# Optimization experiments

Measured on AMD Instinct MI355X. Metric: run time of the kernel, lower is better.

## Reference

```python
import jax, jax.numpy as jnp
import numpy as np
from jax import lax

GRID_N = 80
C_FEAT = 128
HID = 256
NLAYERS = 12


def _make_grid_mesh(n):
    xs = np.linspace(-0.9, 0.9, n, dtype=np.float32)
    X, Y = np.meshgrid(xs, xs, indexing='xy')
    verts = np.stack([X.ravel(), Y.ravel(), np.zeros(n * n, np.float32)], 1)
    idx = np.arange(n * n).reshape(n, n)
    a = idx[:-1, :-1].ravel(); b = idx[:-1, 1:].ravel()
    c = idx[1:, :-1].ravel(); d = idx[1:, 1:].ravel()
    faces = np.concatenate([np.stack([a, b, c], 1), np.stack([b, d, c], 1)], 0)
    return verts, faces.astype(np.int64)


def _edges_and_inv(faces):
    F = faces.shape[0]
    e = np.concatenate([faces[:, [0, 1]], faces[:, [1, 2]], faces[:, [2, 0]]], 0)
    e = np.sort(e, 1)
    edges, inv = np.unique(e, axis=0, return_inverse=True)
    inv = inv.reshape(-1)
    return edges.astype(np.int32), inv[:F], inv[F:2 * F], inv[2 * F:]


def _subdivide_faces(faces, V):
    # new vertex k is midpoint of unique edge k, placed at index V + k
    edges, i01, i12, i20 = _edges_and_inv(faces)
    m01 = V + i01; m12 = V + i12; m20 = V + i20
    v0, v1, v2 = faces[:, 0], faces[:, 1], faces[:, 2]
    nf = np.concatenate([np.stack([v0, m01, m20], 1), np.stack([v1, m12, m01], 1),
                         np.stack([v2, m20, m12], 1), np.stack([m01, m12, m20], 1)], 0)
    return edges, nf


def _topology():
    verts0, f1 = _make_grid_mesh(GRID_N)
    V1 = verts0.shape[0]
    edges1, f2 = _subdivide_faces(f1, V1)
    V2 = V1 + edges1.shape[0]
    edges2, f3 = _subdivide_faces(f2, V2)
    V3 = V2 + edges2.shape[0]
    edges3 = _edges_and_inv(f3)[0]
    return verts0, edges1, edges2, edges3, V3


def _vert_align(feat, verts):
    # feat [C,H,W]; sample bilinearly at vertex (x,y) in [-1,1], align_corners, zero padding
    C, H, W = feat.shape
    fx = (verts[:, 0] + 1.0) * 0.5 * (W - 1)
    fy = (verts[:, 1] + 1.0) * 0.5 * (H - 1)
    x0 = jnp.floor(fx); y0 = jnp.floor(fy)
    wx = fx - x0; wy = fy - y0
    x0i = x0.astype(jnp.int32); y0i = y0.astype(jnp.int32)
    fT = jnp.transpose(feat, (1, 2, 0))  # [H,W,C]

    def samp(yi, xi):
        valid = ((yi >= 0) & (yi < H) & (xi >= 0) & (xi < W)).astype(feat.dtype)
        v = fT[jnp.clip(yi, 0, H - 1), jnp.clip(xi, 0, W - 1)]
        return v * valid[:, None]

    return (samp(y0i, x0i) * ((1 - wy) * (1 - wx))[:, None]
            + samp(y0i, x0i + 1) * ((1 - wy) * wx)[:, None]
            + samp(y0i + 1, x0i) * (wy * (1 - wx))[:, None]
            + samp(y0i + 1, x0i + 1) * (wy * wx)[:, None])


def _gconv(x, e0, e1, w, b):
    # pytorch3d GraphConv: w0(x) + sum_{j in N(i)} w1(x_j), undirected edges
    h0 = x @ w[0] + b[0]
    h1 = x @ w[1] + b[1]
    agg = jnp.zeros_like(h0).at[e0].add(h1[e1]).at[e1].add(h1[e0])
    return h0 + agg


def _stage(feat, edges, w_in, b_in, w_h, b_h, w_out, b_out):
    e0, e1 = edges[:, 0], edges[:, 1]
    x = _gconv(feat, e0, e1, w_in, b_in)

    def body(xc, p):
        return _gconv(xc, e0, e1, p[0], p[1]), None

    x, _ = lax.scan(body, x, (w_h, b_h))
    coords = _gconv(x, e0, e1, w_out, b_out)
    return x, coords


def _subdiv(f, edges):
    # SubdivideMeshes feature/vertex rule: append edge midpoints
    return jnp.concatenate([f, 0.5 * (f[edges[:, 0]] + f[edges[:, 1]])], 0)


def setup_inputs() -> dict:
    key = jax.random.key(0)
    ks = jax.random.split(key, 16)
    verts0, edges1, edges2, edges3, V3 = _topology()

    def pw(k, din, dout, L=None):
        shape = (L, 2, din, dout) if L else (2, din, dout)
        return jax.random.normal(k, shape, dtype=jnp.float32) / np.float32(np.sqrt(7.0 * din))

    din2 = C_FEAT + HID
    inp = {
        'conv64': jax.random.normal(ks[0], (C_FEAT, 56, 56), jnp.float32),
        'conv128': jax.random.normal(ks[1], (C_FEAT, 28, 28), jnp.float32),
        'conv256': jax.random.normal(ks[2], (C_FEAT, 14, 14), jnp.float32),
        'verts0': jnp.asarray(verts0),
        'edges1': jnp.asarray(edges1), 'edges2': jnp.asarray(edges2), 'edges3': jnp.asarray(edges3),
        'w_in1': pw(ks[3], C_FEAT, HID), 'b_in1': jnp.zeros((2, HID), jnp.float32),
        'w_h1': pw(ks[4], HID, HID, NLAYERS), 'b_h1': jnp.zeros((NLAYERS, 2, HID), jnp.float32),
        'w_out1': pw(ks[5], HID, 3), 'b_out1': jnp.zeros((2, 3), jnp.float32),
        'w_in2': pw(ks[6], din2, HID), 'b_in2': jnp.zeros((2, HID), jnp.float32),
        'w_h2': pw(ks[7], HID, HID, NLAYERS), 'b_h2': jnp.zeros((NLAYERS, 2, HID), jnp.float32),
        'w_out2': pw(ks[8], HID, 3), 'b_out2': jnp.zeros((2, 3), jnp.float32),
        'w_in3': pw(ks[9], din2, HID), 'b_in3': jnp.zeros((2, HID), jnp.float32),
        'w_h3': pw(ks[10], HID, HID, NLAYERS), 'b_h3': jnp.zeros((NLAYERS, 2, HID), jnp.float32),
        'w_out3': pw(ks[11], HID, 3), 'b_out3': jnp.zeros((2, 3), jnp.float32),
    }
    return inp


def reference(conv64, conv128, conv256, verts0,
              w_in1, b_in1, w_h1, b_h1, w_out1, b_out1,
              w_in2, b_in2, w_h2, b_h2, w_out2, b_out2,
              w_in3, b_in3, w_h3, b_h3, w_out3, b_out3,
              edges1, edges2, edges3):
    # stage 1: vert_align on conv64 + 14 graph convs -> coords
    x, c1 = _stage(_vert_align(conv64, verts0), edges1, w_in1, b_in1, w_h1, b_h1, w_out1, b_out1)
    v2 = _subdiv(c1, edges1)
    h2 = _subdiv(x, edges1)
    f2 = jnp.concatenate([_vert_align(conv128, v2), h2], 1)
    x, c2 = _stage(f2, edges2, w_in2, b_in2, w_h2, b_h2, w_out2, b_out2)
    v3 = _subdiv(c2, edges2)
    h3 = _subdiv(x, edges2)
    f3 = jnp.concatenate([_vert_align(conv256, v3), h3], 1)
    _, c3 = _stage(f3, edges3, w_in3, b_in3, w_h3, b_h3, w_out3, b_out3)
    return c3
```

## Files before the change

kernel.cpp:

```cpp
#include <hip/hip_runtime.h>
#include <utility>

#define HID 256

typedef __attribute__((ext_vector_type(8))) short bf16x8;
typedef __attribute__((ext_vector_type(4))) float f32x4;
typedef __attribute__((ext_vector_type(4))) unsigned short us4;
typedef __attribute__((ext_vector_type(8))) unsigned short us8;

constexpr size_t MAXN3 = 100489;
constexpr size_t MAXE3 = 300200;

constexpr size_t OFF_IN1 = 0;
constexpr size_t OFF_IN2 = OFF_IN1 + 2 * 256 * 128;
constexpr size_t OFF_IN3 = OFF_IN2 + 2 * 256 * 384;
constexpr size_t OFF_H1  = OFF_IN3 + 2 * 256 * 384;
constexpr size_t OFF_H2  = OFF_H1 + 24 * 256 * 256;
constexpr size_t OFF_H3  = OFF_H2 + 24 * 256 * 256;
constexpr size_t WT_TOTAL = OFF_H3 + 24 * 256 * 256;

__device__ __attribute__((aligned(16))) unsigned short g_Ah[MAXN3 * 256];
__device__ __attribute__((aligned(16))) unsigned short g_Al[MAXN3 * 256];
__device__ __attribute__((aligned(16))) unsigned short g_Bh[MAXN3 * 256];
__device__ __attribute__((aligned(16))) unsigned short g_Bl[MAXN3 * 256];
__device__ __attribute__((aligned(16))) unsigned short g_Gh[MAXN3 * 256];
__device__ __attribute__((aligned(16))) unsigned short g_Gl[MAXN3 * 256];
__device__ __attribute__((aligned(16))) unsigned short g_Dh[MAXN3 * 256];
__device__ __attribute__((aligned(16))) unsigned short g_Dl[MAXN3 * 256];
__device__ __attribute__((aligned(16))) unsigned short g_VAh[MAXN3 * 128];
__device__ __attribute__((aligned(16))) unsigned short g_VAl[MAXN3 * 128];
__device__ float g_C0[MAXN3 * 3];
__device__ float g_C2[MAXN3 * 3];
__device__ float g_Vv[MAXN3 * 3];
__device__ float g_T [56 * 56 * 128];
__device__ __attribute__((aligned(16))) unsigned short g_Wth[WT_TOTAL];
__device__ __attribute__((aligned(16))) unsigned short g_Wtl[WT_TOTAL];
__device__ int g_deg   [MAXN3];
__device__ int g_rowptr[MAXN3 + 1];
__device__ int g_cursor[MAXN3];
__device__ int g_adj   [2 * MAXE3];
__device__ int g_bsum  [128];

__device__ inline float b2f(unsigned short h) {
  return __uint_as_float((unsigned)h << 16);
}
__device__ inline void fsplit(float f, unsigned short& h, unsigned short& l) {
  unsigned u = __float_as_uint(f);
  h = (unsigned short)(u >> 16);
  float hf = __uint_as_float(u & 0xffff0000u);
  l = (unsigned short)(__float_as_uint(f - hf) >> 16);
}

#define GLOAD16(g, l)                                                       \
  __builtin_amdgcn_global_load_lds(                                        \
      (const __attribute__((address_space(1))) unsigned*)(const void*)(g), \
      (__attribute__((address_space(3))) unsigned*)(void*)(l), 16, 0, 0)

__global__ __launch_bounds__(256) void k_wtrans(const float* __restrict__ W,
                                                unsigned short* __restrict__ Oh,
                                                unsigned short* __restrict__ Ol,
                                                int K) {
  __shared__ float Ls[64][65];
  int ktb = blockIdx.x, cb = blockIdx.y, mat = blockIdx.z;
  int nktb = gridDim.x;
  const float* Wm = W + (size_t)mat * K * 256;
  int t = threadIdx.x;
#pragma unroll
  for (int i = 0; i < 16; ++i) {
    int idx = i * 256 + t;
    int kk = idx >> 6, cc = idx & 63;
    Ls[kk][cc] = Wm[(size_t)(ktb * 64 + kk) * 256 + cb * 64 + cc];
  }
  __syncthreads();
  size_t tb = ((size_t)(mat * 4 + cb) * nktb + ktb) * 4096;
#pragma unroll
  for (int i = 0; i < 2; ++i) {
    int c = t * 2 + i;
    int n = c >> 3, sp = c & 7;
    int kbase = (sp ^ (n & 7)) * 8;
    unsigned short hb[8], lb[8];
#pragma unroll
    for (int j = 0; j < 8; ++j) {
      float v = Ls[kbase + j][n];
      unsigned short hi, lo;
      fsplit(v, hi, lo);
      hb[j] = hi;
      lb[j] = lo;
    }
    *(us4*)(Oh + tb + c * 8)     = (us4){hb[0], hb[1], hb[2], hb[3]};
    *(us4*)(Oh + tb + c * 8 + 4) = (us4){hb[4], hb[5], hb[6], hb[7]};
    *(us4*)(Ol + tb + c * 8)     = (us4){lb[0], lb[1], lb[2], lb[3]};
    *(us4*)(Ol + tb + c * 8 + 4) = (us4){lb[4], lb[5], lb[6], lb[7]};
  }
}


__global__ __launch_bounds__(256) void k_count(const int* __restrict__ edges,
                                               int* __restrict__ deg, int E) {
  int e = blockIdx.x * blockDim.x + threadIdx.x;
  if (e >= E) return;
  atomicAdd(&deg[edges[2 * e + 0]], 1);
  atomicAdd(&deg[edges[2 * e + 1]], 1);
}

__global__ __launch_bounds__(256) void k_scan_part(const int* __restrict__ deg,
                                                   int* __restrict__ bsum, int N) {
  __shared__ int s[256];
  int t = threadIdx.x;
  int base = blockIdx.x * 1024 + t * 4;
  int v = 0;
#pragma unroll
  for (int i = 0; i < 4; ++i) {
    int idx = base + i;
    if (idx < N) v += deg[idx];
  }
  s[t] = v;
  __syncthreads();
  for (int off = 128; off > 0; off >>= 1) {
    if (t < off) s[t] += s[t + off];
    __syncthreads();
  }
  if (t == 0) bsum[blockIdx.x] = s[0];
}

__global__ __launch_bounds__(128) void k_scan_top(int* __restrict__ bsum, int nb) {
  __shared__ int s[128];
  int t = threadIdx.x;
  s[t] = (t < nb) ? bsum[t] : 0;
  __syncthreads();
  for (int off = 1; off < 128; off <<= 1) {
    int v = (t >= off) ? s[t - off] : 0;
    __syncthreads();
    s[t] += v;
    __syncthreads();
  }
  if (t < nb) bsum[t] = (t == 0) ? 0 : s[t - 1];
}

__global__ __launch_bounds__(256) void k_scan_write(const int* __restrict__ deg,
                                                    const int* __restrict__ bsum,
                                                    int* __restrict__ rowptr,
                                                    int* __restrict__ cursor, int N) {
  __shared__ int s[256];
  int t = threadIdx.x;
  int base = blockIdx.x * 1024;
  int d[4];
  int local = 0;
#pragma unroll
  for (int i = 0; i < 4; ++i) {
    int idx = base + t * 4 + i;
    d[i] = (idx < N) ? deg[idx] : 0;
    local += d[i];
  }
  s[t] = local;
  __syncthreads();
  for (int off = 1; off < 256; off <<= 1) {
    int v = (t >= off) ? s[t - off] : 0;
    __syncthreads();
    s[t] += v;
    __syncthreads();
  }
  int run = bsum[blockIdx.x] + s[t] - local;
#pragma unroll
  for (int i = 0; i < 4; ++i) {
    int idx = base + t * 4 + i;
    if (idx < N) {
      rowptr[idx] = run;
      cursor[idx] = run;
    }
    run += d[i];
  }
  if (blockIdx.x == gridDim.x - 1 && t == 255) rowptr[N] = run;
}

__global__ __launch_bounds__(256) void k_fill(const int* __restrict__ edges,
                                              int* __restrict__ cursor,
                                              int* __restrict__ adj, int E) {
  int e = blockIdx.x * blockDim.x + threadIdx.x;
  if (e >= E) return;
  int a = edges[2 * e + 0];
  int b = edges[2 * e + 1];
  adj[atomicAdd(&cursor[a], 1)] = b;
  adj[atomicAdd(&cursor[b], 1)] = a;
}


__global__ __launch_bounds__(128) void k_transpose(const float* __restrict__ in,
                                                   float* __restrict__ out, int HW) {
  int p = blockIdx.x;
  int c = threadIdx.x;
  if (p < HW) out[(size_t)p * 128 + c] = in[(size_t)c * HW + p];
}

__global__ __launch_bounds__(128) void k_vert_align(const float* __restrict__ fT,
                                                    const float* __restrict__ verts,
                                                    unsigned short* __restrict__ oh,
                                                    unsigned short* __restrict__ ol,
                                                    int N, int H, int W) {
  int v = blockIdx.x;
  if (v >= N) return;
  int c = threadIdx.x;
  float vx = verts[(size_t)v * 3 + 0];
  float vy = verts[(size_t)v * 3 + 1];
  float fx = (vx + 1.f) * 0.5f * (float)(W - 1);
  float fy = (vy + 1.f) * 0.5f * (float)(H - 1);
  float x0f = floorf(fx), y0f = floorf(fy);
  float wx = fx - x0f, wy = fy - y0f;
  int x0 = (int)x0f, y0 = (int)y0f;
  float acc = 0.f;
#pragma unroll
  for (int dy = 0; dy < 2; ++dy) {
#pragma unroll
    for (int dx = 0; dx < 2; ++dx) {
      int yi = y0 + dy, xi = x0 + dx;
      bool valid = (yi >= 0) && (yi < H) && (xi >= 0) && (xi < W);
      int yc = min(max(yi, 0), H - 1);
      int xc = min(max(xi, 0), W - 1);
      float val = fT[((size_t)yc * W + xc) * 128 + c];
      float wgt = (dy ? wy : 1.f - wy) * (dx ? wx : 1.f - wx);
      acc += valid ? val * wgt : 0.f;
    }
  }
  unsigned short h, l;
  fsplit(acc, h, l);
  oh[(size_t)v * 128 + c] = h;
  ol[(size_t)v * 128 + c] = l;
}

template <int CH>
__global__ __launch_bounds__(256) void k_gather(const int* __restrict__ rowptr,
                                                const int* __restrict__ adj,
                                                const unsigned short* __restrict__ Xh,
                                                const unsigned short* __restrict__ Xl,
                                                unsigned short* __restrict__ Gh,
                                                unsigned short* __restrict__ Gl, int N) {
  constexpr int TPV = CH / 8;
  int idx = blockIdx.x * blockDim.x + threadIdx.x;
  int v = idx / TPV;
  if (v >= N) return;
  int c = (idx % TPV) * 8;
  float a[8] = {};
  int lo = rowptr[v], hi = rowptr[v + 1];
  for (int i = lo; i < hi; ++i) {
    size_t base = (size_t)adj[i] * CH + c;
    us8 h = *(const us8*)(Xh + base);
    us8 l = *(const us8*)(Xl + base);
#pragma unroll
    for (int j = 0; j < 8; ++j) a[j] += b2f(h[j]) + b2f(l[j]);
  }
  us8 oh, ol;
#pragma unroll
  for (int j = 0; j < 8; ++j) {
    unsigned short hh, ll;
    fsplit(a[j], hh, ll);
    oh[j] = hh;
    ol[j] = ll;
  }
  *(us8*)(Gh + (size_t)v * CH + c) = oh;
  *(us8*)(Gl + (size_t)v * CH + c) = ol;
}

struct Panels {
  const unsigned short* ph[4];
  const unsigned short* pl[4];
  int ks[4];
  int ld[4];
};

#define SWZ(row, slot) (((row) * 64) + (((slot) ^ ((row) & 7)) << 3))

__global__ __launch_bounds__(256, 2) void k_layer(
    Panels pd, int Kmm,
    const unsigned short* __restrict__ w0h, const unsigned short* __restrict__ w0l,
    const unsigned short* __restrict__ w1h, const unsigned short* __restrict__ w1l,
    int Kw,
    const float* __restrict__ b0, const float* __restrict__ b1,
    const int* __restrict__ deg,
    unsigned short* __restrict__ Yh, unsigned short* __restrict__ Yl, int N) {
  __shared__ __attribute__((aligned(16))) unsigned short Xh_lds[128 * 64];
  __shared__ __attribute__((aligned(16))) unsigned short Xl_lds[128 * 64];
  __shared__ __attribute__((aligned(16))) unsigned short Wh_lds[2 * 4096];
  __shared__ __attribute__((aligned(16))) unsigned short Wl_lds[2 * 4096];
  int tid = threadIdx.x;
  int lane = tid & 63;
  int wid = tid >> 6;
  int wm = wid >> 1;
  int wn = wid & 1;

  int nrt = (N + 127) >> 7;
  int total = nrt * 2;
  int flat = blockIdx.x;
  int rowtile, colblk;
  if ((flat & ~15) + 16 <= total) {
    int sub = flat & 15;
    rowtile = (flat >> 4) * 8 + (sub & 7);
    colblk = sub >> 3;
  } else {
    rowtile = flat >> 1;
    colblk = flat & 1;
  }
  int row0 = rowtile * 128;
  int col0 = colblk * 128;
  int nktbw = Kw >> 6;

  f32x4 acc[4][4];
#pragma unroll
  for (int m = 0; m < 4; ++m)
#pragma unroll
    for (int n = 0; n < 4; ++n) acc[m][n] = (f32x4){0.f, 0.f, 0.f, 0.f};

  for (int kt = 0; kt < Kmm; kt += 64) {
    int pi = (kt >= pd.ks[1]) + (kt >= pd.ks[2]) + (kt >= pd.ks[3]);
    const unsigned short* bph = pd.ph[pi];
    const unsigned short* bpl = pd.pl[pi];
    int ld = pd.ld[pi];
    int koff = kt - pd.ks[pi];
#pragma unroll
    for (int i = 0; i < 4; ++i) {
      int c = (wid * 4 + i) * 64 + lane;
      int row = c >> 3, slot = c & 7;
      int vg = min(row0 + row, N - 1);
      size_t so = (size_t)vg * ld + koff + ((slot ^ (row & 7)) << 3);
      GLOAD16(bph + so, &Xh_lds[(size_t)c * 8]);
      GLOAD16(bpl + so, &Xl_lds[(size_t)c * 8]);
    }
    {
      int ktb = (kt < Kw) ? (kt >> 6) : ((kt - Kw) >> 6);
      const unsigned short* mh = (kt < Kw) ? w0h : w1h;
      const unsigned short* ml = (kt < Kw) ? w0l : w1l;
#pragma unroll
      for (int i = 0; i < 4; ++i) {
        int c = (wid * 4 + i) * 64 + lane;
        int half = c >> 9, ci = c & 511;
        size_t tb = ((size_t)((2 * colblk + half) * nktbw + ktb)) * 4096 + (size_t)ci * 8;
        GLOAD16(mh + tb, &Wh_lds[half * 4096 + ci * 8]);
        GLOAD16(ml + tb, &Wl_lds[half * 4096 + ci * 8]);
      }
    }
    __syncthreads();
#pragma unroll
    for (int ks = 0; ks < 2; ++ks) {
      int slot = ks * 4 + (lane >> 4);
      bf16x8 ah[4], al[4];
#pragma unroll
      for (int m = 0; m < 4; ++m) {
        int row = wm * 64 + m * 16 + (lane & 15);
        int off = SWZ(row, slot);
        ah[m] = *(const bf16x8*)&Xh_lds[off];
        al[m] = *(const bf16x8*)&Xl_lds[off];
      }
      bf16x8 bh[4], bl[4];
#pragma unroll
      for (int n = 0; n < 4; ++n) {
        int nr = n * 16 + (lane & 15);
        int off = wn * 4096 + SWZ(nr, slot);
        bh[n] = *(const bf16x8*)&Wh_lds[off];
        bl[n] = *(const bf16x8*)&Wl_lds[off];
      }
#pragma unroll
      for (int m = 0; m < 4; ++m)
#pragma unroll
        for (int n = 0; n < 4; ++n) {
          f32x4 c = acc[m][n];
          c = __builtin_amdgcn_mfma_f32_16x16x32_bf16(al[m], bh[n], c, 0, 0, 0);
          c = __builtin_amdgcn_mfma_f32_16x16x32_bf16(ah[m], bl[n], c, 0, 0, 0);
          c = __builtin_amdgcn_mfma_f32_16x16x32_bf16(ah[m], bh[n], c, 0, 0, 0);
          acc[m][n] = c;
        }
    }
    __syncthreads();
  }

#pragma unroll
  for (int m = 0; m < 4; ++m) {
    int rbase = row0 + wm * 64 + m * 16 + (lane >> 4) * 4;
    float dv[4];
#pragma unroll
    for (int r = 0; r < 4; ++r)
      dv[r] = (rbase + r < N) ? (float)deg[rbase + r] : 0.f;
#pragma unroll
    for (int n = 0; n < 4; ++n) {
      int col = col0 + wn * 64 + n * 16 + (lane & 15);
      float bb0 = b0[col], bb1 = b1[col];
      f32x4 v = acc[m][n];
#pragma unroll
      for (int r = 0; r < 4; ++r) {
        int row = rbase + r;
        if (row < N) {
          unsigned short h, l;
          fsplit(v[r] + bb0 + dv[r] * bb1, h, l);
          Yh[(size_t)row * HID + col] = h;
          Yl[(size_t)row * HID + col] = l;
        }
      }
    }
  }
}

__global__ __launch_bounds__(256) void k_rowdot6(const unsigned short* __restrict__ Xh,
                                                 const unsigned short* __restrict__ Xl,
                                                 const float* __restrict__ W,
                                                 const float* __restrict__ b,
                                                 float* __restrict__ Y0,
                                                 float* __restrict__ Y1, int N) {
  int gid = blockIdx.x * blockDim.x + threadIdx.x;
  int row = gid >> 6;
  int lane = threadIdx.x & 63;
  if (row >= N) return;
  size_t base = (size_t)row * HID + lane * 4;
  us4 hv = *(const us4*)(Xh + base);
  us4 lv = *(const us4*)(Xl + base);
  float s[6] = {0.f, 0.f, 0.f, 0.f, 0.f, 0.f};
#pragma unroll
  for (int k = 0; k < 4; ++k) {
    float x = b2f(hv[k]) + b2f(lv[k]);
    int kk = lane * 4 + k;
#pragma unroll
    for (int j = 0; j < 3; ++j) {
      s[j]     += x * W[kk * 3 + j];
      s[3 + j] += x * W[768 + kk * 3 + j];
    }
  }
#pragma unroll
  for (int off = 32; off > 0; off >>= 1)
#pragma unroll
    for (int j = 0; j < 6; ++j) s[j] += __shfl_down(s[j], off);
  if (lane == 0) {
#pragma unroll
    for (int j = 0; j < 3; ++j) {
      Y0[(size_t)row * 3 + j] = s[j] + b[j];
      Y1[(size_t)row * 3 + j] = s[3 + j] + b[3 + j];
    }
  }
}

__global__ __launch_bounds__(256) void k_scatter3(const int* __restrict__ edges,
                                                  const float* __restrict__ H,
                                                  float* __restrict__ OUT, int E) {
  int e = blockIdx.x * blockDim.x + threadIdx.x;
  if (e >= E) return;
  int a = edges[(size_t)e * 2 + 0];
  int b = edges[(size_t)e * 2 + 1];
#pragma unroll
  for (int k = 0; k < 3; ++k) {
    atomicAdd(&OUT[(size_t)a * 3 + k], H[(size_t)b * 3 + k]);
    atomicAdd(&OUT[(size_t)b * 3 + k], H[(size_t)a * 3 + k]);
  }
}

__global__ __launch_bounds__(256) void k_subdiv3(const float* __restrict__ c,
                                                 const int* __restrict__ edges,
                                                 float* __restrict__ v, int N, int E) {
  int i = blockIdx.x * blockDim.x + threadIdx.x;
  if (i >= N + E) return;
  if (i < N) {
#pragma unroll
    for (int k = 0; k < 3; ++k) v[(size_t)i * 3 + k] = c[(size_t)i * 3 + k];
  } else {
    int e = i - N;
    int a = edges[(size_t)e * 2 + 0];
    int b = edges[(size_t)e * 2 + 1];
#pragma unroll
    for (int k = 0; k < 3; ++k)
      v[(size_t)i * 3 + k] = 0.5f * (c[(size_t)a * 3 + k] + c[(size_t)b * 3 + k]);
  }
}

__global__ __launch_bounds__(256) void k_subdiv_feat(const unsigned short* __restrict__ xh,
                                                     const unsigned short* __restrict__ xl,
                                                     const int* __restrict__ edges,
                                                     unsigned short* __restrict__ oh,
                                                     unsigned short* __restrict__ ol,
                                                     int N, int E) {
  int idx = blockIdx.x * blockDim.x + threadIdx.x;
  int v = idx >> 5;
  if (v >= N + E) return;
  int c = (idx & 31) * 8;
  us8 rh, rl;
  if (v < N) {
    rh = *(const us8*)(xh + (size_t)v * HID + c);
    rl = *(const us8*)(xl + (size_t)v * HID + c);
  } else {
    int e = v - N;
    int a = edges[(size_t)e * 2 + 0];
    int b = edges[(size_t)e * 2 + 1];
    us8 ahv = *(const us8*)(xh + (size_t)a * HID + c);
    us8 alv = *(const us8*)(xl + (size_t)a * HID + c);
    us8 bhv = *(const us8*)(xh + (size_t)b * HID + c);
    us8 blv = *(const us8*)(xl + (size_t)b * HID + c);
#pragma unroll
    for (int j = 0; j < 8; ++j) {
      float f = 0.5f * ((b2f(ahv[j]) + b2f(alv[j])) + (b2f(bhv[j]) + b2f(blv[j])));
      unsigned short hh, ll;
      fsplit(f, hh, ll);
      rh[j] = hh;
      rl[j] = ll;
    }
  }
  *(us8*)(oh + (size_t)v * HID + c) = rh;
  *(us8*)(ol + (size_t)v * HID + c) = rl;
}


extern "C" void kernel_launch(void* const* d_in, const int* in_sizes, int n_in,
                              void* d_out, int out_size, void* d_ws, size_t ws_size,
                              hipStream_t stream) {
  const float* conv64  = (const float*)d_in[0];
  const float* conv128 = (const float*)d_in[1];
  const float* conv256 = (const float*)d_in[2];
  const float* verts0  = (const float*)d_in[3];
  const int*   edges1  = (const int*)d_in[4];
  const int*   edges2  = (const int*)d_in[5];
  const int*   edges3  = (const int*)d_in[6];
  const float* w_in1 = (const float*)d_in[7],  *b_in1 = (const float*)d_in[8];
  const float* w_h1  = (const float*)d_in[9],  *b_h1  = (const float*)d_in[10];
  const float* w_out1= (const float*)d_in[11], *b_out1= (const float*)d_in[12];
  const float* w_in2 = (const float*)d_in[13], *b_in2 = (const float*)d_in[14];
  const float* w_h2  = (const float*)d_in[15], *b_h2  = (const float*)d_in[16];
  const float* w_out2= (const float*)d_in[17], *b_out2= (const float*)d_in[18];
  const float* w_in3 = (const float*)d_in[19], *b_in3 = (const float*)d_in[20];
  const float* w_h3  = (const float*)d_in[21], *b_h3  = (const float*)d_in[22];
  const float* w_out3= (const float*)d_in[23], *b_out3= (const float*)d_in[24];

  const int N1 = in_sizes[3] / 3;
  const int E1 = in_sizes[4] / 2;
  const int E2 = in_sizes[5] / 2;
  const int E3 = in_sizes[6] / 2;
  const int N2 = N1 + E1;
  const int N3 = N2 + E2;
  if ((size_t)N3 > MAXN3 || (size_t)E3 > MAXE3) return;

  unsigned short *Ah, *Al, *Bh, *Bl, *Gh, *Gl, *Dh, *Dl, *VAh, *VAl;
  float *C0, *C2, *Vv, *T;
  unsigned short *Wth, *Wtl;
  int *deg, *rowptr, *cursor, *adj, *bsum;
  hipGetSymbolAddress((void**)&Ah,  HIP_SYMBOL(g_Ah));
  hipGetSymbolAddress((void**)&Al,  HIP_SYMBOL(g_Al));
  hipGetSymbolAddress((void**)&Bh,  HIP_SYMBOL(g_Bh));
  hipGetSymbolAddress((void**)&Bl,  HIP_SYMBOL(g_Bl));
  hipGetSymbolAddress((void**)&Gh,  HIP_SYMBOL(g_Gh));
  hipGetSymbolAddress((void**)&Gl,  HIP_SYMBOL(g_Gl));
  hipGetSymbolAddress((void**)&Dh,  HIP_SYMBOL(g_Dh));
  hipGetSymbolAddress((void**)&Dl,  HIP_SYMBOL(g_Dl));
  hipGetSymbolAddress((void**)&VAh, HIP_SYMBOL(g_VAh));
  hipGetSymbolAddress((void**)&VAl, HIP_SYMBOL(g_VAl));
  hipGetSymbolAddress((void**)&C0, HIP_SYMBOL(g_C0));
  hipGetSymbolAddress((void**)&C2, HIP_SYMBOL(g_C2));
  hipGetSymbolAddress((void**)&Vv, HIP_SYMBOL(g_Vv));
  hipGetSymbolAddress((void**)&T,  HIP_SYMBOL(g_T));
  hipGetSymbolAddress((void**)&Wth, HIP_SYMBOL(g_Wth));
  hipGetSymbolAddress((void**)&Wtl, HIP_SYMBOL(g_Wtl));
  hipGetSymbolAddress((void**)&deg,    HIP_SYMBOL(g_deg));
  hipGetSymbolAddress((void**)&rowptr, HIP_SYMBOL(g_rowptr));
  hipGetSymbolAddress((void**)&cursor, HIP_SYMBOL(g_cursor));
  hipGetSymbolAddress((void**)&adj,    HIP_SYMBOL(g_adj));
  hipGetSymbolAddress((void**)&bsum,   HIP_SYMBOL(g_bsum));

  k_wtrans<<<dim3(2, 4, 2),  256, 0, stream>>>(w_in1, Wth + OFF_IN1, Wtl + OFF_IN1, 128);
  k_wtrans<<<dim3(6, 4, 2),  256, 0, stream>>>(w_in2, Wth + OFF_IN2, Wtl + OFF_IN2, 384);
  k_wtrans<<<dim3(6, 4, 2),  256, 0, stream>>>(w_in3, Wth + OFF_IN3, Wtl + OFF_IN3, 384);
  k_wtrans<<<dim3(4, 4, 24), 256, 0, stream>>>(w_h1,  Wth + OFF_H1,  Wtl + OFF_H1,  256);
  k_wtrans<<<dim3(4, 4, 24), 256, 0, stream>>>(w_h2,  Wth + OFF_H2,  Wtl + OFF_H2,  256);
  k_wtrans<<<dim3(4, 4, 24), 256, 0, stream>>>(w_h3,  Wth + OFF_H3,  Wtl + OFF_H3,  256);

  const int BIG = 0x7fffffff;

  auto layerGrid = [](int N) { return dim3((unsigned)(((N + 127) / 128) * 2)); };

  auto build_csr = [&](const int* edges, int E, int N) {
    hipMemsetAsync(deg, 0, (size_t)N * sizeof(int), stream);
    k_count<<<(E + 255) / 256, 256, 0, stream>>>(edges, deg, E);
    int nb = (N + 1023) / 1024;
    k_scan_part<<<nb, 256, 0, stream>>>(deg, bsum, N);
    k_scan_top<<<1, 128, 0, stream>>>(bsum, nb);
    k_scan_write<<<nb, 256, 0, stream>>>(deg, bsum, rowptr, cursor, N);
    k_fill<<<(E + 255) / 256, 256, 0, stream>>>(edges, cursor, adj, E);
  };

  auto gconv_hidden = [&](size_t offH, const float* bh, int N) {
    unsigned short *Xh = Ah, *Xl = Al, *Yh = Bh, *Yl = Bl;
    for (int l = 0; l < 12; ++l) {
      const unsigned short* w0h = Wth + offH + (size_t)(2 * l + 0) * 65536;
      const unsigned short* w0l = Wtl + offH + (size_t)(2 * l + 0) * 65536;
      const unsigned short* w1h = Wth + offH + (size_t)(2 * l + 1) * 65536;
      const unsigned short* w1l = Wtl + offH + (size_t)(2 * l + 1) * 65536;
      const float* b0 = bh + (size_t)l * 2 * HID;
      const float* b1 = b0 + HID;
      k_gather<256><<<((size_t)N * 32 + 255) / 256, 256, 0, stream>>>(
          rowptr, adj, Xh, Xl, Gh, Gl, N);
      Panels pd = {{Xh, Gh, nullptr, nullptr}, {Xl, Gl, nullptr, nullptr},
                   {0, 256, BIG, BIG}, {256, 256, 0, 0}};
      k_layer<<<layerGrid(N), 256, 0, stream>>>(pd, 512, w0h, w0l, w1h, w1l, 256,
                                                b0, b1, deg, Yh, Yl, N);
      std::swap(Xh, Yh);
      std::swap(Xl, Yl);
    }
  };

  auto gconv_out = [&](const unsigned short* Xh, const unsigned short* Xl,
                       const float* wo, const float* bo,
                       float* Cdst, const int* edges, int E, int N) {
    k_rowdot6<<<((size_t)N * 64 + 255) / 256, 256, 0, stream>>>(Xh, Xl, wo, bo, Cdst, C2, N);
    k_scatter3<<<(E + 255) / 256, 256, 0, stream>>>(edges, C2, Cdst, E);
  };

  build_csr(edges1, E1, N1);
  k_transpose<<<56 * 56, 128, 0, stream>>>(conv64, T, 56 * 56);
  k_vert_align<<<N1, 128, 0, stream>>>(T, verts0, VAh, VAl, N1, 56, 56);
  k_gather<128><<<((size_t)N1 * 16 + 255) / 256, 256, 0, stream>>>(
      rowptr, adj, VAh, VAl, Gh, Gl, N1);
  {
    Panels pd = {{VAh, Gh, nullptr, nullptr}, {VAl, Gl, nullptr, nullptr},
                 {0, 128, BIG, BIG}, {128, 128, 0, 0}};
    k_layer<<<layerGrid(N1), 256, 0, stream>>>(pd, 256,
        Wth + OFF_IN1, Wtl + OFF_IN1, Wth + OFF_IN1 + 32768, Wtl + OFF_IN1 + 32768, 128,
        b_in1, b_in1 + HID, deg, Ah, Al, N1);
  }
  gconv_hidden(OFF_H1, b_h1, N1);
  gconv_out(Ah, Al, w_out1, b_out1, C0, edges1, E1, N1);
  k_subdiv3<<<(N2 + 255) / 256, 256, 0, stream>>>(C0, edges1, Vv, N1, E1);
  k_subdiv_feat<<<((size_t)N2 * 32 + 255) / 256, 256, 0, stream>>>(
      Ah, Al, edges1, Dh, Dl, N1, E1);

  build_csr(edges2, E2, N2);
  k_transpose<<<28 * 28, 128, 0, stream>>>(conv128, T, 28 * 28);
  k_vert_align<<<N2, 128, 0, stream>>>(T, Vv, VAh, VAl, N2, 28, 28);
  k_gather<128><<<((size_t)N2 * 16 + 255) / 256, 256, 0, stream>>>(
      rowptr, adj, VAh, VAl, Gh, Gl, N2);
  k_gather<256><<<((size_t)N2 * 32 + 255) / 256, 256, 0, stream>>>(
      rowptr, adj, Dh, Dl, Bh, Bl, N2);
  {
    const size_t m0 = OFF_IN2, m1 = OFF_IN2 + (size_t)256 * 384;
    Panels pd = {{VAh, Dh, Gh, Bh}, {VAl, Dl, Gl, Bl},
                 {0, 128, 384, 512}, {128, 256, 128, 256}};
    k_layer<<<layerGrid(N2), 256, 0, stream>>>(pd, 768,
        Wth + m0, Wtl + m0, Wth + m1, Wtl + m1, 384,
        b_in2, b_in2 + HID, deg, Ah, Al, N2);
  }
  gconv_hidden(OFF_H2, b_h2, N2);
  gconv_out(Ah, Al, w_out2, b_out2, C0, edges2, E2, N2);
  k_subdiv3<<<(N3 + 255) / 256, 256, 0, stream>>>(C0, edges2, Vv, N2, E2);
  k_subdiv_feat<<<((size_t)N3 * 32 + 255) / 256, 256, 0, stream>>>(
      Ah, Al, edges2, Dh, Dl, N2, E2);

  build_csr(edges3, E3, N3);
  k_transpose<<<14 * 14, 128, 0, stream>>>(conv256, T, 14 * 14);
  k_vert_align<<<N3, 128, 0, stream>>>(T, Vv, VAh, VAl, N3, 14, 14);
  k_gather<128><<<((size_t)N3 * 16 + 255) / 256, 256, 0, stream>>>(
      rowptr, adj, VAh, VAl, Gh, Gl, N3);
  k_gather<256><<<((size_t)N3 * 32 + 255) / 256, 256, 0, stream>>>(
      rowptr, adj, Dh, Dl, Bh, Bl, N3);
  {
    const size_t m0 = OFF_IN3, m1 = OFF_IN3 + (size_t)256 * 384;
    Panels pd = {{VAh, Dh, Gh, Bh}, {VAl, Dl, Gl, Bl},
                 {0, 128, 384, 512}, {128, 256, 128, 256}};
    k_layer<<<layerGrid(N3), 256, 0, stream>>>(pd, 768,
        Wth + m0, Wtl + m0, Wth + m1, Wtl + m1, 384,
        b_in3, b_in3 + HID, deg, Ah, Al, N3);
  }
  gconv_hidden(OFF_H3, b_h3, N3);
  float* OUT = (float*)d_out;
  k_rowdot6<<<((size_t)N3 * 64 + 255) / 256, 256, 0, stream>>>(
      Ah, Al, w_out3, b_out3, OUT, C2, N3);
  k_scatter3<<<(E3 + 255) / 256, 256, 0, stream>>>(edges3, C2, OUT, E3);
}
```

Baseline: 4.070 ms.

## Double-buffer GEMM LDS tiles with K=32 steps and matching weight layout

The layer GEMM now runs K in 32-wide steps with two LDS buffers, so the async global-to-LDS loads for the next tile are issued before computing on the current one, and one barrier per step replaces two. The weight pre-transform kernel is rewritten to emit 32-wide K blocks with a new 4-slot swizzle that matches the smaller tile. Total LDS use stays the same. The trade is half as many MFMAs per barrier and a changed swizzle pattern that could add bank conflicts.

```diff
diff --git a/kernel.cpp b/kernel.cpp
--- a/kernel.cpp
+++ b/kernel.cpp
@@ -60,38 +60,35 @@
                                                 unsigned short* __restrict__ Oh,
                                                 unsigned short* __restrict__ Ol,
                                                 int K) {
-  __shared__ float Ls[64][65];
+  __shared__ float Ls[32][65];
   int ktb = blockIdx.x, cb = blockIdx.y, mat = blockIdx.z;
   int nktb = gridDim.x;
   const float* Wm = W + (size_t)mat * K * 256;
   int t = threadIdx.x;
 #pragma unroll
-  for (int i = 0; i < 16; ++i) {
+  for (int i = 0; i < 8; ++i) {
     int idx = i * 256 + t;
     int kk = idx >> 6, cc = idx & 63;
-    Ls[kk][cc] = Wm[(size_t)(ktb * 64 + kk) * 256 + cb * 64 + cc];
+    Ls[kk][cc] = Wm[(size_t)(ktb * 32 + kk) * 256 + cb * 64 + cc];
   }
   __syncthreads();
-  size_t tb = ((size_t)(mat * 4 + cb) * nktb + ktb) * 4096;
-#pragma unroll
-  for (int i = 0; i < 2; ++i) {
-    int c = t * 2 + i;
-    int n = c >> 3, sp = c & 7;
-    int kbase = (sp ^ (n & 7)) * 8;
-    unsigned short hb[8], lb[8];
-#pragma unroll
-    for (int j = 0; j < 8; ++j) {
-      float v = Ls[kbase + j][n];
-      unsigned short hi, lo;
-      fsplit(v, hi, lo);
-      hb[j] = hi;
-      lb[j] = lo;
-    }
-    *(us4*)(Oh + tb + c * 8)     = (us4){hb[0], hb[1], hb[2], hb[3]};
-    *(us4*)(Oh + tb + c * 8 + 4) = (us4){hb[4], hb[5], hb[6], hb[7]};
-    *(us4*)(Ol + tb + c * 8)     = (us4){lb[0], lb[1], lb[2], lb[3]};
-    *(us4*)(Ol + tb + c * 8 + 4) = (us4){lb[4], lb[5], lb[6], lb[7]};
-  }
+  size_t tb = ((size_t)(mat * 4 + cb) * nktb + ktb) * 2048;
+  int c = t;
+  int n = c >> 2, sp = c & 3;
+  int kbase = (sp ^ ((n >> 1) & 3)) * 8;
+  unsigned short hb[8], lb[8];
+#pragma unroll
+  for (int j = 0; j < 8; ++j) {
+    float v = Ls[kbase + j][n];
+    unsigned short hi, lo;
+    fsplit(v, hi, lo);
+    hb[j] = hi;
+    lb[j] = lo;
+  }
+  *(us4*)(Oh + tb + c * 8)     = (us4){hb[0], hb[1], hb[2], hb[3]};
+  *(us4*)(Oh + tb + c * 8 + 4) = (us4){hb[4], hb[5], hb[6], hb[7]};
+  *(us4*)(Ol + tb + c * 8)     = (us4){lb[0], lb[1], lb[2], lb[3]};
+  *(us4*)(Ol + tb + c * 8 + 4) = (us4){lb[4], lb[5], lb[6], lb[7]};
 }
 
 
@@ -267,7 +264,7 @@
   int ld[4];
 };
 
-#define SWZ(row, slot) (((row) * 64) + (((slot) ^ ((row) & 7)) << 3))
+#define SWZ32(row, slot) (((row) * 32) + (((slot) ^ (((row) >> 1) & 3)) << 3))
 
 __global__ __launch_bounds__(256, 2) void k_layer(
     Panels pd, int Kmm,
@@ -277,10 +274,10 @@
     const float* __restrict__ b0, const float* __restrict__ b1,
     const int* __restrict__ deg,
     unsigned short* __restrict__ Yh, unsigned short* __restrict__ Yl, int N) {
-  __shared__ __attribute__((aligned(16))) unsigned short Xh_lds[128 * 64];
-  __shared__ __attribute__((aligned(16))) unsigned short Xl_lds[128 * 64];
-  __shared__ __attribute__((aligned(16))) unsigned short Wh_lds[2 * 4096];
-  __shared__ __attribute__((aligned(16))) unsigned short Wl_lds[2 * 4096];
+  __shared__ __attribute__((aligned(16))) unsigned short Xh_lds[2][128 * 32];
+  __shared__ __attribute__((aligned(16))) unsigned short Xl_lds[2][128 * 32];
+  __shared__ __attribute__((aligned(16))) unsigned short Wh_lds[2][2 * 2048];
+  __shared__ __attribute__((aligned(16))) unsigned short Wl_lds[2][2 * 2048];
   int tid = threadIdx.x;
   int lane = tid & 63;
   int wid = tid >> 6;
@@ -301,7 +298,7 @@
   }
   int row0 = rowtile * 128;
   int col0 = colblk * 128;
-  int nktbw = Kw >> 6;
+  int nktbw = Kw >> 5;
 
   f32x4 acc[4][4];
 #pragma unroll
@@ -309,66 +306,73 @@
 #pragma unroll
     for (int n = 0; n < 4; ++n) acc[m][n] = (f32x4){0.f, 0.f, 0.f, 0.f};
 
-  for (int kt = 0; kt < Kmm; kt += 64) {
+  auto STAGE = [&](int buf, int kt) {
     int pi = (kt >= pd.ks[1]) + (kt >= pd.ks[2]) + (kt >= pd.ks[3]);
     const unsigned short* bph = pd.ph[pi];
     const unsigned short* bpl = pd.pl[pi];
     int ld = pd.ld[pi];
     int koff = kt - pd.ks[pi];
 #pragma unroll
-    for (int i = 0; i < 4; ++i) {
-      int c = (wid * 4 + i) * 64 + lane;
-      int row = c >> 3, slot = c & 7;
+    for (int i = 0; i < 2; ++i) {
+      int c = (wid * 2 + i) * 64 + lane;
+      int row = c >> 2, slot = c & 3;
       int vg = min(row0 + row, N - 1);
-      size_t so = (size_t)vg * ld + koff + ((slot ^ (row & 7)) << 3);
-      GLOAD16(bph + so, &Xh_lds[(size_t)c * 8]);
-      GLOAD16(bpl + so, &Xl_lds[(size_t)c * 8]);
-    }
-    {
-      int ktb = (kt < Kw) ? (kt >> 6) : ((kt - Kw) >> 6);
-      const unsigned short* mh = (kt < Kw) ? w0h : w1h;
-      const unsigned short* ml = (kt < Kw) ? w0l : w1l;
-#pragma unroll
-      for (int i = 0; i < 4; ++i) {
-        int c = (wid * 4 + i) * 64 + lane;
-        int half = c >> 9, ci = c & 511;
-        size_t tb = ((size_t)((2 * colblk + half) * nktbw + ktb)) * 4096 + (size_t)ci * 8;
-        GLOAD16(mh + tb, &Wh_lds[half * 4096 + ci * 8]);
-        GLOAD16(ml + tb, &Wl_lds[half * 4096 + ci * 8]);
+      size_t so = (size_t)vg * ld + koff + ((slot ^ ((row >> 1) & 3)) << 3);
+      GLOAD16(bph + so, &Xh_lds[buf][(size_t)c * 8]);
+      GLOAD16(bpl + so, &Xl_lds[buf][(size_t)c * 8]);
+    }
+    int ktb = (kt < Kw) ? (kt >> 5) : ((kt - Kw) >> 5);
+    const unsigned short* mh = (kt < Kw) ? w0h : w1h;
+    const unsigned short* ml = (kt < Kw) ? w0l : w1l;
+#pragma unroll
+    for (int i = 0; i < 2; ++i) {
+      int c = (wid * 2 + i) * 64 + lane;
+      int half = c >> 8, ci = c & 255;
+      size_t tb = ((size_t)((2 * colblk + half) * nktbw + ktb)) * 2048 + (size_t)ci * 8;
+      GLOAD16(mh + tb, &Wh_lds[buf][(size_t)c * 8]);
+      GLOAD16(ml + tb, &Wl_lds[buf][(size_t)c * 8]);
+    }
+  };
+
+  auto COMPUTE = [&](int buf) {
+    int slot = lane >> 4;
+    bf16x8 ah[4], al[4];
+#pragma unroll
+    for (int m = 0; m < 4; ++m) {
+      int row = wm * 64 + m * 16 + (lane & 15);
+      int off = SWZ32(row, slot);
+      ah[m] = *(const bf16x8*)&Xh_lds[buf][off];
+      al[m] = *(const bf16x8*)&Xl_lds[buf][off];
+    }
+    bf16x8 bh[4], bl[4];
+#pragma unroll
+    for (int n = 0; n < 4; ++n) {
+      int nr = n * 16 + (lane & 15);
+      int off = wn * 2048 + SWZ32(nr, slot);
+      bh[n] = *(const bf16x8*)&Wh_lds[buf][off];
+      bl[n] = *(const bf16x8*)&Wl_lds[buf][off];
+    }
+#pragma unroll
+    for (int m = 0; m < 4; ++m)
+#pragma unroll
+      for (int n = 0; n < 4; ++n) {
+        f32x4 c = acc[m][n];
+        c = __builtin_amdgcn_mfma_f32_16x16x32_bf16(al[m], bh[n], c, 0, 0, 0);
+        c = __builtin_amdgcn_mfma_f32_16x16x32_bf16(ah[m], bl[n], c, 0, 0, 0);
+        c = __builtin_amdgcn_mfma_f32_16x16x32_bf16(ah[m], bh[n], c, 0, 0, 0);
+        acc[m][n] = c;
       }
-    }
+  };
+
+  int nt = Kmm >> 5;
+  STAGE(0, 0);
+  __syncthreads();
+  int buf = 0;
+  for (int t = 0; t < nt; ++t) {
+    if (t + 1 < nt) STAGE(buf ^ 1, (t + 1) << 5);
+    COMPUTE(buf);
     __syncthreads();
-#pragma unroll
-    for (int ks = 0; ks < 2; ++ks) {
-      int slot = ks * 4 + (lane >> 4);
-      bf16x8 ah[4], al[4];
-#pragma unroll
-      for (int m = 0; m < 4; ++m) {
-        int row = wm * 64 + m * 16 + (lane & 15);
-        int off = SWZ(row, slot);
-        ah[m] = *(const bf16x8*)&Xh_lds[off];
-        al[m] = *(const bf16x8*)&Xl_lds[off];
-      }
-      bf16x8 bh[4], bl[4];
-#pragma unroll
-      for (int n = 0; n < 4; ++n) {
-        int nr = n * 16 + (lane & 15);
-        int off = wn * 4096 + SWZ(nr, slot);
-        bh[n] = *(const bf16x8*)&Wh_lds[off];
-        bl[n] = *(const bf16x8*)&Wl_lds[off];
-      }
-#pragma unroll
-      for (int m = 0; m < 4; ++m)
-#pragma unroll
-        for (int n = 0; n < 4; ++n) {
-          f32x4 c = acc[m][n];
-          c = __builtin_amdgcn_mfma_f32_16x16x32_bf16(al[m], bh[n], c, 0, 0, 0);
-          c = __builtin_amdgcn_mfma_f32_16x16x32_bf16(ah[m], bl[n], c, 0, 0, 0);
-          c = __builtin_amdgcn_mfma_f32_16x16x32_bf16(ah[m], bh[n], c, 0, 0, 0);
-          acc[m][n] = c;
-        }
-    }
-    __syncthreads();
+    buf ^= 1;
   }
 
 #pragma unroll
@@ -556,12 +560,12 @@
   hipGetSymbolAddress((void**)&adj,    HIP_SYMBOL(g_adj));
   hipGetSymbolAddress((void**)&bsum,   HIP_SYMBOL(g_bsum));
 
-  k_wtrans<<<dim3(2, 4, 2),  256, 0, stream>>>(w_in1, Wth + OFF_IN1, Wtl + OFF_IN1, 128);
-  k_wtrans<<<dim3(6, 4, 2),  256, 0, stream>>>(w_in2, Wth + OFF_IN2, Wtl + OFF_IN2, 384);
-  k_wtrans<<<dim3(6, 4, 2),  256, 0, stream>>>(w_in3, Wth + OFF_IN3, Wtl + OFF_IN3, 384);
-  k_wtrans<<<dim3(4, 4, 24), 256, 0, stream>>>(w_h1,  Wth + OFF_H1,  Wtl + OFF_H1,  256);
-  k_wtrans<<<dim3(4, 4, 24), 256, 0, stream>>>(w_h2,  Wth + OFF_H2,  Wtl + OFF_H2,  256);
-  k_wtrans<<<dim3(4, 4, 24), 256, 0, stream>>>(w_h3,  Wth + OFF_H3,  Wtl + OFF_H3,  256);
+  k_wtrans<<<dim3(4, 4, 2),   256, 0, stream>>>(w_in1, Wth + OFF_IN1, Wtl + OFF_IN1, 128);
+  k_wtrans<<<dim3(12, 4, 2),  256, 0, stream>>>(w_in2, Wth + OFF_IN2, Wtl + OFF_IN2, 384);
+  k_wtrans<<<dim3(12, 4, 2),  256, 0, stream>>>(w_in3, Wth + OFF_IN3, Wtl + OFF_IN3, 384);
+  k_wtrans<<<dim3(8, 4, 24),  256, 0, stream>>>(w_h1,  Wth + OFF_H1,  Wtl + OFF_H1,  256);
+  k_wtrans<<<dim3(8, 4, 24),  256, 0, stream>>>(w_h2,  Wth + OFF_H2,  Wtl + OFF_H2,  256);
+  k_wtrans<<<dim3(8, 4, 24),  256, 0, stream>>>(w_h3,  Wth + OFF_H3,  Wtl + OFF_H3,  256);
 
   const int BIG = 0x7fffffff;
 
```

Measured after the change: 4.376 ms. 1.08x slower.
